# Kernel optimization log

Measured on AMD Instinct MI355X. Metric: run time of the kernel, lower is better.

The kernel has to match this reference:

```python
import jax, jax.numpy as jnp
import numpy as np

EPS = 1e-5  # haiku LayerNorm default


def _layernorm_last(x, scale, offset):
    m = jnp.mean(x, axis=-1, keepdims=True)
    v = jnp.var(x, axis=-1, keepdims=True)
    return (x - m) * jax.lax.rsqrt(v + EPS) * scale + offset


def setup_inputs() -> dict:
    key = jax.random.key(0)
    ks = jax.random.split(key, 6)
    N, C = 512, 128
    return {
        "act": jax.random.normal(ks[0], (N, N, C), dtype=jnp.float32),
        "mask": jnp.ones((N, N), dtype=jnp.float32),
        "ln_scale": jnp.ones((C,), dtype=jnp.float32),
        "ln_offset": jnp.zeros((C,), dtype=jnp.float32),
        "w_proj": jax.random.normal(ks[1], (C, 2 * C), dtype=jnp.float32) * 0.02,
        "w_gate": jax.random.normal(ks[2], (C, 2 * C), dtype=jnp.float32) * 0.02,
        "cn_scale": jnp.ones((C,), dtype=jnp.float32),
        "cn_offset": jnp.zeros((C,), dtype=jnp.float32),
        "w_out": jax.random.normal(ks[3], (C, C), dtype=jnp.float32) * 0.02,
        "b_out": jnp.zeros((C,), dtype=jnp.float32),
        "w_gate_out": jax.random.normal(ks[4], (C, C), dtype=jnp.float32) * 0.02,
        "b_gate_out": jnp.ones((C,), dtype=jnp.float32),  # bias_init=1.0
    }


def reference(act, mask, ln_scale, ln_offset, w_proj, w_gate,
              cn_scale, cn_offset, w_out, b_out, w_gate_out, b_gate_out):
    C = act.shape[-1]
    # left_norm_input (LayerNorm over channel axis)
    x = _layernorm_last(act, ln_scale, ln_offset)  # [N,N,C]
    input_act = x
    # gated linear unit: projection * sigmoid(gate), no biases (GLU kernel path)
    proj = jnp.einsum('ijc,cd->ijd', x, w_proj) * jax.nn.sigmoid(
        jnp.einsum('ijc,cd->ijd', x, w_gate))  # [N,N,2C]
    proj = jnp.transpose(proj, (2, 0, 1)) * mask[None]  # [2C,N,N]
    # split even/odd channels: reshape(C,2,N,N) -> a=proj[:,0], b=proj[:,1]
    proj = proj.reshape(C, 2, *proj.shape[1:])
    a, b = proj[:, 0], proj[:, 1]  # each [C,N,N]
    # triangle einsum ('ikc,jkc->ijc' -> 'cik,cjk->cij')
    act2 = jnp.einsum('cik,cjk->cij', a, b)  # [C,N,N]
    # center_norm: LayerNorm over channel axis (axis=0), params on axis 0
    m = jnp.mean(act2, axis=0, keepdims=True)
    v = jnp.var(act2, axis=0, keepdims=True)
    act2 = (act2 - m) * jax.lax.rsqrt(v + EPS) * cn_scale[:, None, None] + cn_offset[:, None, None]
    out = jnp.transpose(act2, (1, 2, 0))  # [N,N,C]
    out = jnp.einsum('ijc,cd->ijd', out, w_out) + b_out
    gate_out = jax.nn.sigmoid(jnp.einsum('ijc,cd->ijd', input_act, w_gate_out) + b_gate_out)
    return out * gate_out
```

## Files before the change

### kernel.cpp

```cpp
#include <hip/hip_runtime.h>
#include <stdint.h>

#define NDIM 512
#define CDIM 128
#define MDIM (NDIM*NDIM)

typedef unsigned short u16;
typedef __bf16 bf16v8 __attribute__((ext_vector_type(8)));
typedef float f32x4 __attribute__((ext_vector_type(4)));
typedef short s16x4 __attribute__((ext_vector_type(4)));

__device__ __forceinline__ u16 f2bf(float f){
  union { float f; uint32_t u; } v; v.f = f;
  uint32_t u = v.u;
  u += 0x7fffu + ((u >> 16) & 1u);
  return (u16)(u >> 16);
}
__device__ __forceinline__ float sigm(float x){ return 1.0f/(1.0f + __expf(-x)); }
__device__ __forceinline__ f32x4 mfma_bf16(bf16v8 a, bf16v8 b, f32x4 c){
  return __builtin_amdgcn_mfma_f32_16x16x32_bf16(a, b, c, 0, 0, 0);
}

__global__ void k0_prep(const float* __restrict__ wp, const float* __restrict__ wg,
                        const float* __restrict__ wgo, const float* __restrict__ wo,
                        u16* __restrict__ wt){
  const int d = blockIdx.x, k = threadIdx.x;
  float v;
  if (d < 256)      v = wp[k*256 + d];
  else if (d < 512) v = wg[k*256 + (d-256)];
  else if (d < 640) v = wgo[k*128 + (d-512)];
  else              v = wo[k*128 + (d-640)];
  wt[d*CDIM + k] = f2bf(v);
}

__global__ __launch_bounds__(256) void k1_ln_proj(
    const float* __restrict__ act, const float* __restrict__ mask,
    const float* __restrict__ lns, const float* __restrict__ lno,
    const float* __restrict__ bgo, const u16* __restrict__ wt,
    u16* __restrict__ AB, float* __restrict__ gate)
{
  __shared__ __align__(16) u16 xs[64][136];
  __shared__ __align__(16) u16 pgs[256][72];
  __shared__ float msk[64];
  const int t = threadIdx.x;
  const int m0 = blockIdx.x * 64;

  {
    const int r = t >> 2, q = t & 3;
    const float4* rp = (const float4*)(act + (size_t)(m0 + r)*CDIM + q*32);
    float4 v[8];
    #pragma unroll
    for (int i = 0; i < 8; ++i) v[i] = rp[i];
    float s = 0.f, s2 = 0.f;
    #pragma unroll
    for (int i = 0; i < 8; ++i){
      s  += v[i].x + v[i].y + v[i].z + v[i].w;
      s2 += v[i].x*v[i].x + v[i].y*v[i].y + v[i].z*v[i].z + v[i].w*v[i].w;
    }
    s += __shfl_xor(s, 1);  s2 += __shfl_xor(s2, 1);
    s += __shfl_xor(s, 2);  s2 += __shfl_xor(s2, 2);
    const float mean = s * (1.f/128.f);
    const float rstd = rsqrtf(s2 * (1.f/128.f) - mean*mean + 1e-5f);
    const float4* lsp = (const float4*)(lns + q*32);
    const float4* lop = (const float4*)(lno + q*32);
    #pragma unroll
    for (int i = 0; i < 8; ++i){
      const float4 sc = lsp[i], of = lop[i];
      s16x4 pk;
      pk.x = (short)f2bf((v[i].x - mean)*rstd*sc.x + of.x);
      pk.y = (short)f2bf((v[i].y - mean)*rstd*sc.y + of.y);
      pk.z = (short)f2bf((v[i].z - mean)*rstd*sc.z + of.z);
      pk.w = (short)f2bf((v[i].w - mean)*rstd*sc.w + of.w);
      *(s16x4*)&xs[r][q*32 + i*4] = pk;
    }
    if (t < 64) msk[t] = mask[m0 + t];
  }
  __syncthreads();

  const int w = t >> 6, L = t & 63, ln16 = L & 15, quad = L >> 4;
  bf16v8 af[4][4];
  #pragma unroll
  for (int rs = 0; rs < 4; ++rs)
    #pragma unroll
    for (int kk = 0; kk < 4; ++kk)
      af[rs][kk] = *(const bf16v8*)&xs[rs*16 + ln16][kk*32 + quad*8];

  const f32x4 zero4 = {0.f,0.f,0.f,0.f};
  #pragma unroll
  for (int pp = 0; pp < 4; ++pp){
    const int p = w*4 + pp;
    const u16* wpr = wt + (size_t)(16*p + ln16)*CDIM + quad*8;
    const u16* wgr = wpr + (size_t)256*CDIM;
    bf16v8 bp[4], bg[4];
    #pragma unroll
    for (int kk = 0; kk < 4; ++kk){
      bp[kk] = *(const bf16v8*)(wpr + kk*32);
      bg[kk] = *(const bf16v8*)(wgr + kk*32);
    }
    f32x4 aP[4] = {zero4, zero4, zero4, zero4};
    f32x4 aG[4] = {zero4, zero4, zero4, zero4};
    #pragma unroll
    for (int kk = 0; kk < 4; ++kk)
      #pragma unroll
      for (int rs = 0; rs < 4; ++rs){
        aP[rs] = mfma_bf16(af[rs][kk], bp[kk], aP[rs]);
        aG[rs] = mfma_bf16(af[rs][kk], bg[kk], aG[rs]);
      }
    #pragma unroll
    for (int rs = 0; rs < 4; ++rs)
      #pragma unroll
      for (int reg = 0; reg < 4; ++reg){
        const int ml = rs*16 + quad*4 + reg;
        const float pg = aP[rs][reg] * sigm(aG[rs][reg]) * msk[ml];
        pgs[16*p + ln16][ml] = f2bf(pg);
      }
  }
  #pragma unroll
  for (int u = 0; u < 2; ++u){
    const int e0 = 32*w + 16*u;
    const u16* wr = wt + (size_t)(512 + e0 + ln16)*CDIM + quad*8;
    bf16v8 bb[4];
    #pragma unroll
    for (int kk = 0; kk < 4; ++kk) bb[kk] = *(const bf16v8*)(wr + kk*32);
    f32x4 ag[4] = {zero4, zero4, zero4, zero4};
    #pragma unroll
    for (int kk = 0; kk < 4; ++kk)
      #pragma unroll
      for (int rs = 0; rs < 4; ++rs)
        ag[rs] = mfma_bf16(af[rs][kk], bb[kk], ag[rs]);
    const int e = e0 + ln16;
    const float bias = bgo[e];
    #pragma unroll
    for (int rs = 0; rs < 4; ++rs)
      #pragma unroll
      for (int reg = 0; reg < 4; ++reg){
        const int ml = rs*16 + quad*4 + reg;
        gate[(size_t)(m0 + ml)*CDIM + e] = sigm(ag[rs][reg] + bias);
      }
  }
  __syncthreads();

  #pragma unroll
  for (int p4 = 0; p4 < 4; ++p4){
    const int d = p4*64 + (t >> 2), q = t & 3;
    u16* dst = AB + (size_t)d*MDIM + m0 + q*16;
    const u16* src = &pgs[d][q*16];
    *(bf16v8*)dst       = *(const bf16v8*)src;
    *(bf16v8*)(dst + 8) = *(const bf16v8*)(src + 8);
  }
}

__global__ __launch_bounds__(256) void k2_tri(const u16* __restrict__ AB,
                                              u16* __restrict__ act2)
{
  __shared__ __align__(16) u16 As[128][72];
  __shared__ __align__(16) u16 Bs[128][72];
  const int t = threadIdx.x, bid = blockIdx.x;
  const int c  = bid >> 4;
  const int i0 = ((bid >> 2) & 3) * 128;
  const int j0 = (bid & 3) * 128;
  const u16* Ag = AB + (size_t)(2*c)*MDIM;
  const u16* Bg = AB + (size_t)(2*c + 1)*MDIM;

  const int w = t >> 6, L = t & 63, ln16 = L & 15, quad = L >> 4;
  const int iw = (w & 1)*64, jw = (w >> 1)*64;
  const int r = t >> 1, h = t & 1;

  const f32x4 zero4 = {0.f,0.f,0.f,0.f};
  f32x4 acc[4][4];
  #pragma unroll
  for (int x = 0; x < 4; ++x)
    #pragma unroll
    for (int y = 0; y < 4; ++y) acc[x][y] = zero4;

  for (int k0 = 0; k0 < NDIM; k0 += 64){
    const u16* ga = Ag + (size_t)(i0 + r)*NDIM + k0 + h*32;
    const u16* gb = Bg + (size_t)(j0 + r)*NDIM + k0 + h*32;
    bf16v8 sa[4], sb[4];
    #pragma unroll
    for (int x = 0; x < 4; ++x){
      sa[x] = *(const bf16v8*)(ga + x*8);
      sb[x] = *(const bf16v8*)(gb + x*8);
    }
    __syncthreads();
    #pragma unroll
    for (int x = 0; x < 4; ++x){
      *(bf16v8*)&As[r][h*32 + x*8] = sa[x];
      *(bf16v8*)&Bs[r][h*32 + x*8] = sb[x];
    }
    __syncthreads();
    #pragma unroll
    for (int kk = 0; kk < 2; ++kk){
      bf16v8 ar[4], br[4];
      #pragma unroll
      for (int x = 0; x < 4; ++x) ar[x] = *(const bf16v8*)&As[iw + x*16 + ln16][kk*32 + quad*8];
      #pragma unroll
      for (int y = 0; y < 4; ++y) br[y] = *(const bf16v8*)&Bs[jw + y*16 + ln16][kk*32 + quad*8];
      #pragma unroll
      for (int x = 0; x < 4; ++x)
        #pragma unroll
        for (int y = 0; y < 4; ++y)
          acc[x][y] = mfma_bf16(ar[x], br[y], acc[x][y]);
    }
  }

  u16* op = act2 + (size_t)c*MDIM;
  #pragma unroll
  for (int x = 0; x < 4; ++x)
    #pragma unroll
    for (int y = 0; y < 4; ++y)
      #pragma unroll
      for (int reg = 0; reg < 4; ++reg){
        const int il = iw + x*16 + quad*4 + reg;
        const int jl = jw + y*16 + ln16;
        op[(size_t)(i0 + il)*NDIM + j0 + jl] = f2bf(acc[x][y][reg]);
      }
}

__global__ __launch_bounds__(256) void k3_out(
    const u16* __restrict__ act2, const u16* __restrict__ wt2,
    const float* __restrict__ cns, const float* __restrict__ cno,
    const float* __restrict__ bo, float* __restrict__ out)
{
  __shared__ __align__(16) float vs[128][65];
  __shared__ __align__(16) u16 xs2[64][136];
  __shared__ float csh[128], coh[128];
  const int t = threadIdx.x;
  const int i  = blockIdx.x >> 3;
  const int j0 = (blockIdx.x & 7)*64;
  if (t < 128){ csh[t] = cns[t]; coh[t] = cno[t]; }

  {
    const int cc = t >> 1, h = t & 1;
    const u16* g = act2 + (size_t)cc*MDIM + (size_t)i*NDIM + j0 + h*32;
    #pragma unroll
    for (int x = 0; x < 4; ++x){
      bf16v8 uv = *(const bf16v8*)(g + x*8);
      #pragma unroll
      for (int e = 0; e < 8; ++e) vs[cc][h*32 + x*8 + e] = (float)uv[e];
    }
  }
  __syncthreads();
  {
    const int jj = t >> 2, q = t & 3;
    float s = 0.f, s2 = 0.f;
    #pragma unroll
    for (int ci = 0; ci < 32; ++ci){
      const float v = vs[4*ci + q][jj];
      s += v; s2 += v*v;
    }
    s += __shfl_xor(s,1); s2 += __shfl_xor(s2,1);
    s += __shfl_xor(s,2); s2 += __shfl_xor(s2,2);
    const float mean = s*(1.f/128.f);
    const float rstd = rsqrtf(s2*(1.f/128.f) - mean*mean + 1e-5f);
    #pragma unroll
    for (int ci = 0; ci < 32; ++ci){
      const int cc = 4*ci + q;
      xs2[jj][cc] = f2bf((vs[cc][jj] - mean)*rstd*csh[cc] + coh[cc]);
    }
  }
  __syncthreads();

  const int w = t >> 6, L = t & 63, ln16 = L & 15, quad = L >> 4;
  bf16v8 af[4];
  #pragma unroll
  for (int kk = 0; kk < 4; ++kk)
    af[kk] = *(const bf16v8*)&xs2[w*16 + ln16][kk*32 + quad*8];
  const f32x4 zero4 = {0.f,0.f,0.f,0.f};
  #pragma unroll
  for (int n = 0; n < 8; ++n){
    const u16* wr = wt2 + (size_t)(n*16 + ln16)*CDIM + quad*8;
    bf16v8 bb[4];
    #pragma unroll
    for (int kk = 0; kk < 4; ++kk) bb[kk] = *(const bf16v8*)(wr + kk*32);
    f32x4 ac = zero4;
    #pragma unroll
    for (int kk = 0; kk < 4; ++kk) ac = mfma_bf16(af[kk], bb[kk], ac);
    const int e = n*16 + ln16;
    const float bias = bo[e];
    #pragma unroll
    for (int reg = 0; reg < 4; ++reg){
      const int jl = w*16 + quad*4 + reg;
      const size_t idx = ((size_t)i*NDIM + j0 + jl)*(size_t)CDIM + e;
      out[idx] = (ac[reg] + bias) * out[idx];
    }
  }
}

extern "C" void kernel_launch(void* const* d_in, const int* in_sizes, int n_in,
                              void* d_out, int out_size, void* d_ws, size_t ws_size,
                              hipStream_t stream)
{
  const float* act = (const float*)d_in[0];
  const float* msk = (const float*)d_in[1];
  const float* lns = (const float*)d_in[2];
  const float* lno = (const float*)d_in[3];
  const float* wp  = (const float*)d_in[4];
  const float* wg  = (const float*)d_in[5];
  const float* cns = (const float*)d_in[6];
  const float* cno = (const float*)d_in[7];
  const float* wo  = (const float*)d_in[8];
  const float* bo  = (const float*)d_in[9];
  const float* wgo = (const float*)d_in[10];
  const float* bgo = (const float*)d_in[11];
  float* out = (float*)d_out;

  u16* AB   = (u16*)d_ws;
  u16* ACT2 = AB + (size_t)256*MDIM;
  u16* WT   = ACT2 + (size_t)128*MDIM;

  k0_prep   <<<dim3(768),  dim3(128), 0, stream>>>(wp, wg, wgo, wo, WT);
  k1_ln_proj<<<dim3(4096), dim3(256), 0, stream>>>(act, msk, lns, lno, bgo, WT, AB, out);
  k2_tri    <<<dim3(2048), dim3(256), 0, stream>>>(AB, ACT2);
  k3_out    <<<dim3(4096), dim3(256), 0, stream>>>(ACT2, WT + 640*CDIM, cns, cno, bo, out);
}
```

Before: 546.5 us.

## Repartition k1 warps by row half and column half, with per-warp LDS transpose

Each warp in the LN/projection kernel now handles 32 rows and half of the output channels, instead of all 64 rows and a quarter of the channels. Per-warp double-buffered LDS tiles transpose the gated projection, so stores to AB happen inside the loop and the block-wide barrier and large pgs buffer go away. Mask values are loaded straight into registers, and sigmoid uses a hardware reciprocal. This cuts LDS use and register pressure, which may raise occupancy, but each warp now loads twice as many weight fragments and issues narrower 16-byte global stores.

```diff
diff --git a/kernel.cpp b/kernel.cpp
--- a/kernel.cpp
+++ b/kernel.cpp
@@ -16,7 +16,9 @@
   u += 0x7fffu + ((u >> 16) & 1u);
   return (u16)(u >> 16);
 }
-__device__ __forceinline__ float sigm(float x){ return 1.0f/(1.0f + __expf(-x)); }
+__device__ __forceinline__ float sigm(float x){
+  return __builtin_amdgcn_rcpf(1.0f + __expf(-x));
+}
 __device__ __forceinline__ f32x4 mfma_bf16(bf16v8 a, bf16v8 b, f32x4 c){
   return __builtin_amdgcn_mfma_f32_16x16x32_bf16(a, b, c, 0, 0, 0);
 }
@@ -40,8 +42,7 @@
     u16* __restrict__ AB, float* __restrict__ gate)
 {
   __shared__ __align__(16) u16 xs[64][136];
-  __shared__ __align__(16) u16 pgs[256][72];
-  __shared__ float msk[64];
+  __shared__ __align__(16) u16 pgs[4][2][16][40];
   const int t = threadIdx.x;
   const int m0 = blockIdx.x * 64;
 
@@ -73,23 +74,30 @@
       pk.w = (short)f2bf((v[i].w - mean)*rstd*sc.w + of.w);
       *(s16x4*)&xs[r][q*32 + i*4] = pk;
     }
-    if (t < 64) msk[t] = mask[m0 + t];
   }
   __syncthreads();
 
   const int w = t >> 6, L = t & 63, ln16 = L & 15, quad = L >> 4;
-  bf16v8 af[4][4];
-  #pragma unroll
-  for (int rs = 0; rs < 4; ++rs)
+  const int h = w & 1, u = w >> 1;
+  const int rbase = 32*h;
+
+  bf16v8 af[2][4];
+  #pragma unroll
+  for (int rs = 0; rs < 2; ++rs)
     #pragma unroll
     for (int kk = 0; kk < 4; ++kk)
-      af[rs][kk] = *(const bf16v8*)&xs[rs*16 + ln16][kk*32 + quad*8];
+      af[rs][kk] = *(const bf16v8*)&xs[rbase + rs*16 + ln16][kk*32 + quad*8];
+
+  const float4 mk0 = *(const float4*)(mask + m0 + rbase +      quad*4);
+  const float4 mk1 = *(const float4*)(mask + m0 + rbase + 16 + quad*4);
 
   const f32x4 zero4 = {0.f,0.f,0.f,0.f};
-  #pragma unroll
-  for (int pp = 0; pp < 4; ++pp){
-    const int p = w*4 + pp;
-    const u16* wpr = wt + (size_t)(16*p + ln16)*CDIM + quad*8;
+  const int d2 = L >> 2, mg = L & 3;
+
+  #pragma unroll 2
+  for (int pi = 0; pi < 8; ++pi){
+    const int dg = 128*u + 16*pi;
+    const u16* wpr = wt + (size_t)(dg + ln16)*CDIM + quad*8;
     const u16* wgr = wpr + (size_t)256*CDIM;
     bf16v8 bp[4], bg[4];
     #pragma unroll
@@ -97,56 +105,50 @@
       bp[kk] = *(const bf16v8*)(wpr + kk*32);
       bg[kk] = *(const bf16v8*)(wgr + kk*32);
     }
-    f32x4 aP[4] = {zero4, zero4, zero4, zero4};
-    f32x4 aG[4] = {zero4, zero4, zero4, zero4};
+    f32x4 aP[2] = {zero4, zero4};
+    f32x4 aG[2] = {zero4, zero4};
     #pragma unroll
     for (int kk = 0; kk < 4; ++kk)
       #pragma unroll
-      for (int rs = 0; rs < 4; ++rs){
+      for (int rs = 0; rs < 2; ++rs){
         aP[rs] = mfma_bf16(af[rs][kk], bp[kk], aP[rs]);
         aG[rs] = mfma_bf16(af[rs][kk], bg[kk], aG[rs]);
       }
     #pragma unroll
-    for (int rs = 0; rs < 4; ++rs)
+    for (int rs = 0; rs < 2; ++rs){
+      const float4 mk = rs ? mk1 : mk0;
+      s16x4 pk;
+      pk.x = (short)f2bf(aP[rs][0] * sigm(aG[rs][0]) * mk.x);
+      pk.y = (short)f2bf(aP[rs][1] * sigm(aG[rs][1]) * mk.y);
+      pk.z = (short)f2bf(aP[rs][2] * sigm(aG[rs][2]) * mk.z);
+      pk.w = (short)f2bf(aP[rs][3] * sigm(aG[rs][3]) * mk.w);
+      *(s16x4*)&pgs[w][pi & 1][ln16][rs*16 + quad*4] = pk;
+    }
+    const bf16v8 ov = *(const bf16v8*)&pgs[w][pi & 1][d2][mg*8];
+    *(bf16v8*)(AB + (size_t)(dg + d2)*MDIM + m0 + rbase + mg*8) = ov;
+  }
+
+  #pragma unroll 2
+  for (int n = 0; n < 4; ++n){
+    const int e = 64*u + 16*n + ln16;
+    const u16* wr = wt + (size_t)(512 + e)*CDIM + quad*8;
+    bf16v8 bb[4];
+    #pragma unroll
+    for (int kk = 0; kk < 4; ++kk) bb[kk] = *(const bf16v8*)(wr + kk*32);
+    f32x4 ag[2] = {zero4, zero4};
+    #pragma unroll
+    for (int kk = 0; kk < 4; ++kk)
+      #pragma unroll
+      for (int rs = 0; rs < 2; ++rs)
+        ag[rs] = mfma_bf16(af[rs][kk], bb[kk], ag[rs]);
+    const float bias = bgo[e];
+    #pragma unroll
+    for (int rs = 0; rs < 2; ++rs)
       #pragma unroll
       for (int reg = 0; reg < 4; ++reg){
-        const int ml = rs*16 + quad*4 + reg;
-        const float pg = aP[rs][reg] * sigm(aG[rs][reg]) * msk[ml];
-        pgs[16*p + ln16][ml] = f2bf(pg);
-      }
-  }
-  #pragma unroll
-  for (int u = 0; u < 2; ++u){
-    const int e0 = 32*w + 16*u;
-    const u16* wr = wt + (size_t)(512 + e0 + ln16)*CDIM + quad*8;
-    bf16v8 bb[4];
-    #pragma unroll
-    for (int kk = 0; kk < 4; ++kk) bb[kk] = *(const bf16v8*)(wr + kk*32);
-    f32x4 ag[4] = {zero4, zero4, zero4, zero4};
-    #pragma unroll
-    for (int kk = 0; kk < 4; ++kk)
-      #pragma unroll
-      for (int rs = 0; rs < 4; ++rs)
-        ag[rs] = mfma_bf16(af[rs][kk], bb[kk], ag[rs]);
-    const int e = e0 + ln16;
-    const float bias = bgo[e];
-    #pragma unroll
-    for (int rs = 0; rs < 4; ++rs)
-      #pragma unroll
-      for (int reg = 0; reg < 4; ++reg){
-        const int ml = rs*16 + quad*4 + reg;
+        const int ml = rbase + rs*16 + quad*4 + reg;
         gate[(size_t)(m0 + ml)*CDIM + e] = sigm(ag[rs][reg] + bias);
       }
-  }
-  __syncthreads();
-
-  #pragma unroll
-  for (int p4 = 0; p4 < 4; ++p4){
-    const int d = p4*64 + (t >> 2), q = t & 3;
-    u16* dst = AB + (size_t)d*MDIM + m0 + q*16;
-    const u16* src = &pgs[d][q*16];
-    *(bf16v8*)dst       = *(const bf16v8*)src;
-    *(bf16v8*)(dst + 8) = *(const bf16v8*)(src + 8);
   }
 }
 
```

Result: slower. 599.5 us (+9.7%).

## Move output gate into final kernel, recompute layernorm there, remap triangle block order

Applied to the files above, without the earlier changes.

The gate projection and sigmoid are taken out of the projection kernel, which used to write a full fp32 gate tensor into the output buffer that the last kernel then read back. The last kernel now reloads the raw activations, recomputes the input layernorm and runs the gate matmul itself. This replaces a 128 MB fp32 write plus read with a 128 MB read of the input. The triangle kernel's block index is permuted so neighbouring blocks work on different channels, the staging tile in the output kernel is kept in bf16 to cut LDS use, and the sigmoid now uses a hardware reciprocal.

```diff
diff --git a/kernel.cpp b/kernel.cpp
--- a/kernel.cpp
+++ b/kernel.cpp
@@ -16,7 +16,13 @@
   u += 0x7fffu + ((u >> 16) & 1u);
   return (u16)(u >> 16);
 }
-__device__ __forceinline__ float sigm(float x){ return 1.0f/(1.0f + __expf(-x)); }
+__device__ __forceinline__ float bf2f(u16 h){
+  union { uint32_t u; float f; } v; v.u = ((uint32_t)h) << 16;
+  return v.f;
+}
+__device__ __forceinline__ float sigm(float x){
+  return __builtin_amdgcn_rcpf(1.0f + __expf(-x));
+}
 __device__ __forceinline__ f32x4 mfma_bf16(bf16v8 a, bf16v8 b, f32x4 c){
   return __builtin_amdgcn_mfma_f32_16x16x32_bf16(a, b, c, 0, 0, 0);
 }
@@ -36,8 +42,7 @@
 __global__ __launch_bounds__(256) void k1_ln_proj(
     const float* __restrict__ act, const float* __restrict__ mask,
     const float* __restrict__ lns, const float* __restrict__ lno,
-    const float* __restrict__ bgo, const u16* __restrict__ wt,
-    u16* __restrict__ AB, float* __restrict__ gate)
+    const u16* __restrict__ wt, u16* __restrict__ AB)
 {
   __shared__ __align__(16) u16 xs[64][136];
   __shared__ __align__(16) u16 pgs[256][72];
@@ -115,29 +120,6 @@
         pgs[16*p + ln16][ml] = f2bf(pg);
       }
   }
-  #pragma unroll
-  for (int u = 0; u < 2; ++u){
-    const int e0 = 32*w + 16*u;
-    const u16* wr = wt + (size_t)(512 + e0 + ln16)*CDIM + quad*8;
-    bf16v8 bb[4];
-    #pragma unroll
-    for (int kk = 0; kk < 4; ++kk) bb[kk] = *(const bf16v8*)(wr + kk*32);
-    f32x4 ag[4] = {zero4, zero4, zero4, zero4};
-    #pragma unroll
-    for (int kk = 0; kk < 4; ++kk)
-      #pragma unroll
-      for (int rs = 0; rs < 4; ++rs)
-        ag[rs] = mfma_bf16(af[rs][kk], bb[kk], ag[rs]);
-    const int e = e0 + ln16;
-    const float bias = bgo[e];
-    #pragma unroll
-    for (int rs = 0; rs < 4; ++rs)
-      #pragma unroll
-      for (int reg = 0; reg < 4; ++reg){
-        const int ml = rs*16 + quad*4 + reg;
-        gate[(size_t)(m0 + ml)*CDIM + e] = sigm(ag[rs][reg] + bias);
-      }
-  }
   __syncthreads();
 
   #pragma unroll
@@ -155,7 +137,8 @@
 {
   __shared__ __align__(16) u16 As[128][72];
   __shared__ __align__(16) u16 Bs[128][72];
-  const int t = threadIdx.x, bid = blockIdx.x;
+  const int t = threadIdx.x;
+  const int bid = (blockIdx.x & 7)*256 + (blockIdx.x >> 3);
   const int c  = bid >> 4;
   const int i0 = ((bid >> 2) & 3) * 128;
   const int j0 = (bid & 3) * 128;
@@ -218,26 +201,57 @@
 }
 
 __global__ __launch_bounds__(256) void k3_out(
-    const u16* __restrict__ act2, const u16* __restrict__ wt2,
+    const u16* __restrict__ act2, const u16* __restrict__ wt,
+    const float* __restrict__ act,
+    const float* __restrict__ lns, const float* __restrict__ lno,
     const float* __restrict__ cns, const float* __restrict__ cno,
-    const float* __restrict__ bo, float* __restrict__ out)
+    const float* __restrict__ bo, const float* __restrict__ bgo,
+    float* __restrict__ out)
 {
-  __shared__ __align__(16) float vs[128][65];
+  __shared__ __align__(16) u16 vs[128][72];
   __shared__ __align__(16) u16 xs2[64][136];
+  __shared__ __align__(16) u16 xg[64][136];
   __shared__ float csh[128], coh[128];
   const int t = threadIdx.x;
   const int i  = blockIdx.x >> 3;
   const int j0 = (blockIdx.x & 7)*64;
+  const int m0 = i*NDIM + j0;
   if (t < 128){ csh[t] = cns[t]; coh[t] = cno[t]; }
 
   {
     const int cc = t >> 1, h = t & 1;
     const u16* g = act2 + (size_t)cc*MDIM + (size_t)i*NDIM + j0 + h*32;
     #pragma unroll
-    for (int x = 0; x < 4; ++x){
-      bf16v8 uv = *(const bf16v8*)(g + x*8);
-      #pragma unroll
-      for (int e = 0; e < 8; ++e) vs[cc][h*32 + x*8 + e] = (float)uv[e];
+    for (int x = 0; x < 4; ++x)
+      *(bf16v8*)&vs[cc][h*32 + x*8] = *(const bf16v8*)(g + x*8);
+  }
+  {
+    const int r = t >> 2, q = t & 3;
+    const float4* rp = (const float4*)(act + (size_t)(m0 + r)*CDIM + q*32);
+    float4 v[8];
+    #pragma unroll
+    for (int ii = 0; ii < 8; ++ii) v[ii] = rp[ii];
+    float s = 0.f, s2 = 0.f;
+    #pragma unroll
+    for (int ii = 0; ii < 8; ++ii){
+      s  += v[ii].x + v[ii].y + v[ii].z + v[ii].w;
+      s2 += v[ii].x*v[ii].x + v[ii].y*v[ii].y + v[ii].z*v[ii].z + v[ii].w*v[ii].w;
+    }
+    s += __shfl_xor(s, 1);  s2 += __shfl_xor(s2, 1);
+    s += __shfl_xor(s, 2);  s2 += __shfl_xor(s2, 2);
+    const float mean = s * (1.f/128.f);
+    const float rstd = rsqrtf(s2 * (1.f/128.f) - mean*mean + 1e-5f);
+    const float4* lsp = (const float4*)(lns + q*32);
+    const float4* lop = (const float4*)(lno + q*32);
+    #pragma unroll
+    for (int ii = 0; ii < 8; ++ii){
+      const float4 sc = lsp[ii], of = lop[ii];
+      s16x4 pk;
+      pk.x = (short)f2bf((v[ii].x - mean)*rstd*sc.x + of.x);
+      pk.y = (short)f2bf((v[ii].y - mean)*rstd*sc.y + of.y);
+      pk.z = (short)f2bf((v[ii].z - mean)*rstd*sc.z + of.z);
+      pk.w = (short)f2bf((v[ii].w - mean)*rstd*sc.w + of.w);
+      *(s16x4*)&xg[r][q*32 + ii*4] = pk;
     }
   }
   __syncthreads();
@@ -246,7 +260,7 @@
     float s = 0.f, s2 = 0.f;
     #pragma unroll
     for (int ci = 0; ci < 32; ++ci){
-      const float v = vs[4*ci + q][jj];
+      const float v = bf2f(vs[4*ci + q][jj]);
       s += v; s2 += v*v;
     }
     s += __shfl_xor(s,1); s2 += __shfl_xor(s2,1);
@@ -256,33 +270,42 @@
     #pragma unroll
     for (int ci = 0; ci < 32; ++ci){
       const int cc = 4*ci + q;
-      xs2[jj][cc] = f2bf((vs[cc][jj] - mean)*rstd*csh[cc] + coh[cc]);
+      xs2[jj][cc] = f2bf((bf2f(vs[cc][jj]) - mean)*rstd*csh[cc] + coh[cc]);
     }
   }
   __syncthreads();
 
   const int w = t >> 6, L = t & 63, ln16 = L & 15, quad = L >> 4;
-  bf16v8 af[4];
-  #pragma unroll
-  for (int kk = 0; kk < 4; ++kk)
+  bf16v8 af[4], ag[4];
+  #pragma unroll
+  for (int kk = 0; kk < 4; ++kk){
     af[kk] = *(const bf16v8*)&xs2[w*16 + ln16][kk*32 + quad*8];
+    ag[kk] = *(const bf16v8*)&xg [w*16 + ln16][kk*32 + quad*8];
+  }
   const f32x4 zero4 = {0.f,0.f,0.f,0.f};
   #pragma unroll
   for (int n = 0; n < 8; ++n){
-    const u16* wr = wt2 + (size_t)(n*16 + ln16)*CDIM + quad*8;
-    bf16v8 bb[4];
-    #pragma unroll
-    for (int kk = 0; kk < 4; ++kk) bb[kk] = *(const bf16v8*)(wr + kk*32);
-    f32x4 ac = zero4;
-    #pragma unroll
-    for (int kk = 0; kk < 4; ++kk) ac = mfma_bf16(af[kk], bb[kk], ac);
+    const u16* wr  = wt + (size_t)(640 + n*16 + ln16)*CDIM + quad*8;
+    const u16* wgr = wt + (size_t)(512 + n*16 + ln16)*CDIM + quad*8;
+    bf16v8 bb[4], bg[4];
+    #pragma unroll
+    for (int kk = 0; kk < 4; ++kk){
+      bb[kk] = *(const bf16v8*)(wr  + kk*32);
+      bg[kk] = *(const bf16v8*)(wgr + kk*32);
+    }
+    f32x4 ao = zero4, agg = zero4;
+    #pragma unroll
+    for (int kk = 0; kk < 4; ++kk){
+      ao  = mfma_bf16(af[kk], bb[kk], ao);
+      agg = mfma_bf16(ag[kk], bg[kk], agg);
+    }
     const int e = n*16 + ln16;
-    const float bias = bo[e];
+    const float bias = bo[e], bge = bgo[e];
     #pragma unroll
     for (int reg = 0; reg < 4; ++reg){
       const int jl = w*16 + quad*4 + reg;
-      const size_t idx = ((size_t)i*NDIM + j0 + jl)*(size_t)CDIM + e;
-      out[idx] = (ac[reg] + bias) * out[idx];
+      out[((size_t)(m0 + jl))*(size_t)CDIM + e] =
+          (ao[reg] + bias) * sigm(agg[reg] + bge);
     }
   }
 }
@@ -310,7 +333,8 @@
   u16* WT   = ACT2 + (size_t)128*MDIM;
 
   k0_prep   <<<dim3(768),  dim3(128), 0, stream>>>(wp, wg, wgo, wo, WT);
-  k1_ln_proj<<<dim3(4096), dim3(256), 0, stream>>>(act, msk, lns, lno, bgo, WT, AB, out);
+  k1_ln_proj<<<dim3(4096), dim3(256), 0, stream>>>(act, msk, lns, lno, WT, AB);
   k2_tri    <<<dim3(2048), dim3(256), 0, stream>>>(AB, ACT2);
-  k3_out    <<<dim3(4096), dim3(256), 0, stream>>>(ACT2, WT + 640*CDIM, cns, cno, bo, out);
-}
+  k3_out    <<<dim3(4096), dim3(256), 0, stream>>>(ACT2, WT, act, lns, lno,
+                                                   cns, cno, bo, bgo, out);
+}
```

Result: slower. 564.4 us (+3.3%).
